# Optimization experiments

Measured on AMD Instinct MI355X. Metric: run time of the kernel, lower is better.

## Reference

```python
import jax, jax.numpy as jnp
import numpy as np

EPS = 0.05
THRESH = 1e-6
MAX_ITER = 100


def _l2norm(x):
    # matches torch F.normalize(dim=-1): x / max(||x||, 1e-12)
    n = jnp.sqrt(jnp.sum(x * x, axis=-1, keepdims=True))
    return x / jnp.maximum(n, 1e-12)


def setup_inputs() -> dict:
    key = jax.random.key(0)
    kq, kk, kv = jax.random.split(key, 3)
    B, N, D = 8, 1024, 64
    return {
        "q": jax.random.normal(kq, (B, N, D), dtype=jnp.float32),
        "k": jax.random.normal(kk, (B, N, D), dtype=jnp.float32),
        "V": jax.random.normal(kv, (B, N, D), dtype=jnp.float32),
    }


def reference(q, k, V):
    B, N, D = q.shape
    Q = _l2norm(q)
    Kn = _l2norm(k)
    # cost matrix: 1 - cosine similarity, shape (B, N, N)
    C = 1.0 - jnp.einsum("bnd,bmd->bnm", Q, Kn)

    log_mu = jnp.full((B, N), jnp.log(1.0 / N + 1e-8), dtype=C.dtype)
    log_nu = log_mu

    def kernel(u, v):
        # (-C + u_i + v_j) / eps, shape (B, N, N)
        return (-C + u[:, :, None] + v[:, None, :]) / EPS

    def step(carry, _):
        u, v, done = carry
        u0 = u
        u_new = EPS * (log_mu - jax.scipy.special.logsumexp(kernel(u, v), axis=2)) + u
        v_new = EPS * (log_nu - jax.scipy.special.logsumexp(kernel(u_new, v), axis=1)) + v
        err = jnp.mean(jnp.abs(u_new - u0))
        # replicate torch early-break: once converged, freeze u, v
        u = jnp.where(done, u, u_new)
        v = jnp.where(done, v, v_new)
        done = jnp.logical_or(done, err < THRESH)
        return (u, v, done), None

    u0 = jnp.zeros((B, N), dtype=C.dtype)
    v0 = jnp.zeros((B, N), dtype=C.dtype)
    (u, v, _), _ = jax.lax.scan(
        jax.checkpoint(step), (u0, v0, jnp.array(False)), None, length=MAX_ITER
    )

    T = jnp.exp(kernel(u, v))  # transport plan (B, N, N)
    out = jnp.einsum("bnm,bmd->bnd", T, V) + V
    return out
```

## Files before the change

### kernel.cpp

```cpp
#include <hip/hip_runtime.h>
#include <math.h>

#define BB 8
#define NN 1024
#define DD 64
#define EPSF 0.05f
#define MAX_ITER 100
#define ERR_SUM_THRESH 8.192e-3f
#define SCALE_ 28.853900817779268f
#define EPSLN2_ 0.034657359027997264f
#define NBLK 256
#define NPER 32

typedef __attribute__((ext_vector_type(8))) short short8;
typedef __attribute__((ext_vector_type(4))) float f32x4;

static __device__ __forceinline__ float fexp2(float x) { return __builtin_amdgcn_exp2f(x); }
static __device__ __forceinline__ float flog2(float x) { return __builtin_amdgcn_logf(x); }
static __device__ __forceinline__ float bflo(unsigned u) { return __uint_as_float(u << 16); }
static __device__ __forceinline__ unsigned short bf16rne(float x) {
    unsigned u = __float_as_uint(x);
    u += 0x7fffu + ((u >> 16) & 1u);
    return (unsigned short)(u >> 16);
}
__device__ __forceinline__ float wave_sum64(float x) {
#pragma unroll
    for (int off = 1; off < 64; off <<= 1) x += __shfl_xor(x, off);
    return x;
}

#define ERRIDX(t, b) ((b) * 128 + (t))
#define CNTIDX(p, b) ((b) * 256 + (p))
#define PUBIDX(t) (t)

__global__ __launch_bounds__(256) void cost_kernel(const float* __restrict__ q,
                                                   const float* __restrict__ k,
                                                   unsigned short* __restrict__ M,
                                                   unsigned short* __restrict__ MT) {
    __shared__ __align__(16) float Qs[64][65];
    __shared__ __align__(16) float Ks[64][65];
    __shared__ float qin[64];
    __shared__ float kin[64];
    __shared__ __align__(16) unsigned short Qb[64][72];
    __shared__ __align__(16) unsigned short Kb[64][72];
    int b = blockIdx.z;
    int i0 = blockIdx.y * 64, j0 = blockIdx.x * 64;
    const float* Qp = q + ((size_t)b * NN + i0) * DD;
    const float* Kp = k + ((size_t)b * NN + j0) * DD;
    int tid = threadIdx.x;
#pragma unroll
    for (int kk = 0; kk < 4; ++kk) {
        int c = tid + 256 * kk;
        int row = c >> 4;
        int c4 = c & 15;
        float4 qv = ((const float4*)(Qp + row * DD))[c4];
        Qs[row][c4 * 4 + 0] = qv.x; Qs[row][c4 * 4 + 1] = qv.y;
        Qs[row][c4 * 4 + 2] = qv.z; Qs[row][c4 * 4 + 3] = qv.w;
        float4 kv = ((const float4*)(Kp + row * DD))[c4];
        Ks[row][c4 * 4 + 0] = kv.x; Ks[row][c4 * 4 + 1] = kv.y;
        Ks[row][c4 * 4 + 2] = kv.z; Ks[row][c4 * 4 + 3] = kv.w;
    }
    __syncthreads();
    if (tid < 64) {
        float ss = 0.f;
#pragma unroll 16
        for (int d = 0; d < 64; ++d) ss += Qs[tid][d] * Qs[tid][d];
        qin[tid] = 1.0f / fmaxf(sqrtf(ss), 1e-12f);
    } else if (tid < 128) {
        int r = tid - 64;
        float ss = 0.f;
#pragma unroll 16
        for (int d = 0; d < 64; ++d) ss += Ks[r][d] * Ks[r][d];
        kin[r] = 1.0f / fmaxf(sqrtf(ss), 1e-12f);
    }
    __syncthreads();
    {
        int row = tid >> 2, d0 = (tid & 3) * 16;
        float qs = qin[row], ks = kin[row];
#pragma unroll
        for (int p = 0; p < 4; ++p) {
            int d = d0 + p * 4;
            uint2 t;
            t.x = (unsigned)bf16rne(Qs[row][d + 0] * qs) | ((unsigned)bf16rne(Qs[row][d + 1] * qs) << 16);
            t.y = (unsigned)bf16rne(Qs[row][d + 2] * qs) | ((unsigned)bf16rne(Qs[row][d + 3] * qs) << 16);
            *(uint2*)&Qb[row][d] = t;
            t.x = (unsigned)bf16rne(Ks[row][d + 0] * ks) | ((unsigned)bf16rne(Ks[row][d + 1] * ks) << 16);
            t.y = (unsigned)bf16rne(Ks[row][d + 2] * ks) | ((unsigned)bf16rne(Ks[row][d + 3] * ks) << 16);
            *(uint2*)&Kb[row][d] = t;
        }
    }
    __syncthreads();
    int w = tid >> 6, lane = tid & 63;
    int m = lane & 15, qq = lane >> 4;
    int rloc = w * 16;
    short8 a0 = *(const short8*)&Qb[rloc + m][qq * 8];
    short8 a1 = *(const short8*)&Qb[rloc + m][qq * 8 + 32];
    f32x4 acc[4];
#pragma unroll
    for (int nt = 0; nt < 4; ++nt) {
        short8 b0 = *(const short8*)&Kb[nt * 16 + m][qq * 8];
        short8 b1 = *(const short8*)&Kb[nt * 16 + m][qq * 8 + 32];
        f32x4 z = {0.f, 0.f, 0.f, 0.f};
        z = __builtin_amdgcn_mfma_f32_16x16x32_bf16(a0, b0, z, 0, 0, 0);
        acc[nt] = __builtin_amdgcn_mfma_f32_16x16x32_bf16(a1, b1, z, 0, 0, 0);
    }
#pragma unroll
    for (int nt = 0; nt < 4; ++nt) {
        int gj = j0 + nt * 16 + m;
        unsigned short us[4];
#pragma unroll
        for (int r = 0; r < 4; ++r)
            us[r] = bf16rne(fexp2((acc[nt][r] - 1.0f) * SCALE_));
#pragma unroll
        for (int r = 0; r < 4; ++r)
            M[((size_t)b << 20) + ((size_t)(i0 + rloc + qq * 4 + r) << 10) + gj] = us[r];
        uint2 t;
        t.x = (unsigned)us[0] | ((unsigned)us[1] << 16);
        t.y = (unsigned)us[2] | ((unsigned)us[3] << 16);
        *(uint2*)(MT + ((size_t)b << 20) + ((size_t)gj << 10) + i0 + rloc + qq * 4) = t;
    }
}

#define ACC8(U4, base)                                              \
    s0 = fmaf(bflo(U4.x), wrg[base + 0], s0);                       \
    s1 = fmaf(__uint_as_float(U4.x), wrg[base + 1], s1);            \
    s0 = fmaf(bflo(U4.y), wrg[base + 2], s0);                       \
    s1 = fmaf(__uint_as_float(U4.y), wrg[base + 3], s1);            \
    s0 = fmaf(bflo(U4.z), wrg[base + 4], s0);                       \
    s1 = fmaf(__uint_as_float(U4.z), wrg[base + 5], s1);            \
    s0 = fmaf(bflo(U4.w), wrg[base + 6], s0);                       \
    s1 = fmaf(__uint_as_float(U4.w), wrg[base + 7], s1);

__global__ __launch_bounds__(256, 1) void sink_coop(const unsigned short* __restrict__ M,
                                                    const unsigned short* __restrict__ MT,
                                                    float* __restrict__ u,
                                                    float* __restrict__ v,
                                                    float* __restrict__ err,
                                                    unsigned* __restrict__ cnt,
                                                    unsigned* __restrict__ pub,
                                                    float eln) {
    __shared__ __align__(16) float sw[1280];
    __shared__ float sdel[4];
    __shared__ int sflag;
    int tid = threadIdx.x;
    int w = tid >> 6, lane = tid & 63;
    int b = blockIdx.x & 7;
    int slice = blockIdx.x >> 3;
    int rbase = slice * 32 + w * 8;
    const unsigned short* Mb  = M  + ((size_t)b << 20);
    const unsigned short* MTb = MT + ((size_t)b << 20);
    float* ub = u + (b << 10);
    float* vb = v + (b << 10);

    uint4 mA[8], mB[8], nA[8], nB[8];
#pragma unroll
    for (int r = 0; r < 8; ++r) {
        const uint4* rp = (const uint4*)(Mb + ((size_t)(rbase + r) << 10));
        mA[r] = rp[lane * 2];
        mB[r] = rp[lane * 2 + 1];
        const uint4* tp = (const uint4*)(MTb + ((size_t)(rbase + r) << 10));
        nA[r] = tp[lane * 2];
        nB[r] = tp[lane * 2 + 1];
    }

    float uprev[8];
#pragma unroll
    for (int r = 0; r < 8; ++r) uprev[r] = 0.f;

    for (int t = 0; t < MAX_ITER; ++t) {
        {
            float4 ex;
            ex.x = fexp2(__hip_atomic_load(vb + tid * 4 + 0, __ATOMIC_RELAXED, __HIP_MEMORY_SCOPE_AGENT) * SCALE_);
            ex.y = fexp2(__hip_atomic_load(vb + tid * 4 + 1, __ATOMIC_RELAXED, __HIP_MEMORY_SCOPE_AGENT) * SCALE_);
            ex.z = fexp2(__hip_atomic_load(vb + tid * 4 + 2, __ATOMIC_RELAXED, __HIP_MEMORY_SCOPE_AGENT) * SCALE_);
            ex.w = fexp2(__hip_atomic_load(vb + tid * 4 + 3, __ATOMIC_RELAXED, __HIP_MEMORY_SCOPE_AGENT) * SCALE_);
            *(float4*)&sw[tid * 4 + 4 * (tid >> 2)] = ex;
            __syncthreads();
            float wrg[16];
            *(float4*)&wrg[0]  = *(const float4*)&sw[lane * 20 + 0];
            *(float4*)&wrg[4]  = *(const float4*)&sw[lane * 20 + 4];
            *(float4*)&wrg[8]  = *(const float4*)&sw[lane * 20 + 8];
            *(float4*)&wrg[12] = *(const float4*)&sw[lane * 20 + 12];
            float del = 0.f;
#pragma unroll
            for (int rr = 0; rr < 8; ++rr) {
                float s0 = 0.f, s1 = 0.f;
                ACC8(mA[rr], 0)
                ACC8(mB[rr], 8)
                float s = wave_sum64(s0 + s1);
                float un = eln - EPSLN2_ * flog2(s);
                del += fabsf(un - uprev[rr]);
                uprev[rr] = un;
                if (lane == 0)
                    __hip_atomic_store(ub + rbase + rr, un, __ATOMIC_RELAXED, __HIP_MEMORY_SCOPE_AGENT);
            }
            if (lane == 0) sdel[w] = del;
            asm volatile("s_waitcnt vmcnt(0)" ::: "memory");
            __syncthreads();
            if (tid == 0) {
                __hip_atomic_fetch_add(err + ERRIDX(t, b), sdel[0] + sdel[1] + sdel[2] + sdel[3],
                                       __ATOMIC_RELAXED, __HIP_MEMORY_SCOPE_AGENT);
                asm volatile("s_waitcnt vmcnt(0)" ::: "memory");
                unsigned* c = cnt + CNTIDX(2 * t, b);
                __hip_atomic_fetch_add(c, 1u, __ATOMIC_RELAXED, __HIP_MEMORY_SCOPE_AGENT);
                while (__hip_atomic_load(c, __ATOMIC_RELAXED, __HIP_MEMORY_SCOPE_AGENT) < NPER)
                    __builtin_amdgcn_s_sleep(1);
                if (slice == 0) {
                    asm volatile("s_waitcnt vmcnt(0)" ::: "memory");
                    __hip_atomic_fetch_add(pub + PUBIDX(t), 1u, __ATOMIC_RELAXED, __HIP_MEMORY_SCOPE_AGENT);
                }
            }
            __syncthreads();
        }
        {
            float4 ex;
            ex.x = fexp2(__hip_atomic_load(ub + tid * 4 + 0, __ATOMIC_RELAXED, __HIP_MEMORY_SCOPE_AGENT) * SCALE_);
            ex.y = fexp2(__hip_atomic_load(ub + tid * 4 + 1, __ATOMIC_RELAXED, __HIP_MEMORY_SCOPE_AGENT) * SCALE_);
            ex.z = fexp2(__hip_atomic_load(ub + tid * 4 + 2, __ATOMIC_RELAXED, __HIP_MEMORY_SCOPE_AGENT) * SCALE_);
            ex.w = fexp2(__hip_atomic_load(ub + tid * 4 + 3, __ATOMIC_RELAXED, __HIP_MEMORY_SCOPE_AGENT) * SCALE_);
            *(float4*)&sw[tid * 4 + 4 * (tid >> 2)] = ex;
            __syncthreads();
            float wrg[16];
            *(float4*)&wrg[0]  = *(const float4*)&sw[lane * 20 + 0];
            *(float4*)&wrg[4]  = *(const float4*)&sw[lane * 20 + 4];
            *(float4*)&wrg[8]  = *(const float4*)&sw[lane * 20 + 8];
            *(float4*)&wrg[12] = *(const float4*)&sw[lane * 20 + 12];
#pragma unroll
            for (int rr = 0; rr < 8; ++rr) {
                float s0 = 0.f, s1 = 0.f;
                ACC8(nA[rr], 0)
                ACC8(nB[rr], 8)
                float s = wave_sum64(s0 + s1);
                float vn = eln - EPSLN2_ * flog2(s);
                if (lane == 0)
                    __hip_atomic_store(vb + rbase + rr, vn, __ATOMIC_RELAXED, __HIP_MEMORY_SCOPE_AGENT);
            }
            asm volatile("s_waitcnt vmcnt(0)" ::: "memory");
            __syncthreads();
            if (tid == 0) {
                unsigned* c = cnt + CNTIDX(2 * t + 1, b);
                __hip_atomic_fetch_add(c, 1u, __ATOMIC_RELAXED, __HIP_MEMORY_SCOPE_AGENT);
                while (__hip_atomic_load(c, __ATOMIC_RELAXED, __HIP_MEMORY_SCOPE_AGENT) < NPER)
                    __builtin_amdgcn_s_sleep(1);
                float eb = __hip_atomic_load(err + ERRIDX(t, b), __ATOMIC_RELAXED, __HIP_MEMORY_SCOPE_AGENT);
                int brk = 0;
                if (eb < ERR_SUM_THRESH) {
                    while (__hip_atomic_load(pub + PUBIDX(t), __ATOMIC_RELAXED, __HIP_MEMORY_SCOPE_AGENT) < 8u)
                        __builtin_amdgcn_s_sleep(1);
                    float s = 0.f;
                    for (int bb = 0; bb < 8; ++bb)
                        s += __hip_atomic_load(err + ERRIDX(t, bb), __ATOMIC_RELAXED, __HIP_MEMORY_SCOPE_AGENT);
                    brk = (s < ERR_SUM_THRESH);
                }
                sflag = brk;
            }
            __syncthreads();
            if (sflag) break;
        }
    }
}

__global__ __launch_bounds__(256) void wt_kernel(const float* __restrict__ V,
                                                 const float* __restrict__ v,
                                                 unsigned short* __restrict__ WT) {
    __shared__ __align__(16) float Vs[64][65];
    __shared__ float wj[64];
    int b = blockIdx.x & 7, jt = blockIdx.x >> 3;
    int j0 = jt * 64;
    int tid = threadIdx.x;
    const float* Vb = V + ((size_t)b << 16) + ((size_t)j0 << 6);
#pragma unroll
    for (int c = 0; c < 4; ++c) {
        int idx = tid + 256 * c;
        int row = idx >> 4, c4 = idx & 15;
        float4 x = ((const float4*)(Vb + row * 64))[c4];
        Vs[row][c4 * 4 + 0] = x.x; Vs[row][c4 * 4 + 1] = x.y;
        Vs[row][c4 * 4 + 2] = x.z; Vs[row][c4 * 4 + 3] = x.w;
    }
    if (tid < 64) wj[tid] = fexp2(v[(b << 10) + j0 + tid] * SCALE_);
    __syncthreads();
    int d = tid >> 2, qd = tid & 3;
    unsigned pk[8];
#pragma unroll
    for (int p = 0; p < 8; ++p) {
        int j = qd * 16 + p * 2;
        unsigned lo = bf16rne(Vs[j][d] * wj[j]);
        unsigned hi = bf16rne(Vs[j + 1][d] * wj[j + 1]);
        pk[p] = lo | (hi << 16);
    }
    unsigned short* dst = WT + ((size_t)b << 16) + ((size_t)d << 10) + j0 + qd * 16;
    ((uint4*)dst)[0] = make_uint4(pk[0], pk[1], pk[2], pk[3]);
    ((uint4*)dst)[1] = make_uint4(pk[4], pk[5], pk[6], pk[7]);
}

__global__ __launch_bounds__(256) void gemm_final(const unsigned short* __restrict__ M,
                                                  const unsigned short* __restrict__ WT,
                                                  const float* __restrict__ u,
                                                  const float* __restrict__ V,
                                                  float* __restrict__ out) {
    __shared__ float sa[32];
    int tid = threadIdx.x;
    int w = tid >> 6, lane = tid & 63;
    int b = blockIdx.x & 7, mt = blockIdx.x >> 3;
    if (tid < 32) sa[tid] = fexp2(u[(b << 10) + mt * 32 + tid] * SCALE_);
    __syncthreads();
    int m = lane & 15, q = lane >> 4;
    int rloc = (w & 1) * 16;
    int nbase = (w >> 1) * 32;
    const unsigned short* Ma = M + ((size_t)b << 20) + ((size_t)(mt * 32 + rloc + m) << 10) + q * 8;
    const unsigned short* W0 = WT + ((size_t)b << 16) + ((size_t)(nbase + m) << 10) + q * 8;
    const unsigned short* W1 = W0 + (16 << 10);
    f32x4 acc0 = {0.f, 0.f, 0.f, 0.f}, acc1 = {0.f, 0.f, 0.f, 0.f};
#pragma unroll 4
    for (int k0 = 0; k0 < NN; k0 += 32) {
        short8 af = *(const short8*)(Ma + k0);
        short8 b0 = *(const short8*)(W0 + k0);
        short8 b1 = *(const short8*)(W1 + k0);
        acc0 = __builtin_amdgcn_mfma_f32_16x16x32_bf16(af, b0, acc0, 0, 0, 0);
        acc1 = __builtin_amdgcn_mfma_f32_16x16x32_bf16(af, b1, acc1, 0, 0, 0);
    }
#pragma unroll
    for (int r = 0; r < 4; ++r) {
        int lrow = rloc + q * 4 + r;
        int gm = mt * 32 + lrow;
        float a = sa[lrow];
        size_t base = (((size_t)b << 10) + gm) * DD;
        int n0 = nbase + m;
        out[base + n0]      = fmaf(a, acc0[r], V[base + n0]);
        out[base + n0 + 16] = fmaf(a, acc1[r], V[base + n0 + 16]);
    }
}

extern "C" void kernel_launch(void* const* d_in, const int* in_sizes, int n_in,
                              void* d_out, int out_size, void* d_ws, size_t ws_size,
                              hipStream_t stream) {
    const float* q = (const float*)d_in[0];
    const float* k = (const float*)d_in[1];
    const float* V = (const float*)d_in[2];
    float* out = (float*)d_out;

    char* ws = (char*)d_ws;
    const size_t MB16 = (size_t)BB * NN * NN * sizeof(unsigned short);
    unsigned short* M  = (unsigned short*)ws;
    unsigned short* MT = (unsigned short*)(ws + MB16);
    unsigned short* WT = MT;
    float* u   = (float*)(ws + 2 * MB16);
    float* v   = u + BB * NN;
    float* err = v + BB * NN;
    unsigned* cnt = (unsigned*)(err + 1024);
    unsigned* pub = cnt + 2048;

    size_t zbytes = (size_t)(2 * BB * NN + 1024 + 2048 + 128) * 4;
    hipMemsetAsync(u, 0, zbytes, stream);

    cost_kernel<<<dim3(16, 16, 8), 256, 0, stream>>>(q, k, M, MT);

    float eln = EPSF * logf(1.0f / NN + 1e-8f);
    sink_coop<<<dim3(NBLK), dim3(256), 0, stream>>>(M, MT, u, v, err, cnt, pub, eln);

    wt_kernel<<<128, 256, 0, stream>>>(V, v, WT);
    gemm_final<<<256, 256, 0, stream>>>(M, WT, u, V, out);
}
```

Measured before the change: 196.3 us.

## Pack barrier count and fixed-point error into one 64-bit atomic, coalesce M stores

The per-iteration grid barrier in the Sinkhorn loop now packs the arrival count and a fixed-point error sum into a single 64-bit atomic. This removes the separate error atomic, its waitcnt, and the publish counter, so the convergence check reads per-batch totals directly from the barrier words. The cost kernel also stages the M tile in shared memory and writes it out with coalesced 16-byte stores instead of scattered 2-byte stores. The fixed-point quantisation of the error (scaled by 2^20, plus 1 per block) slightly changes the break threshold semantics.

```diff
diff --git a/kernel.cpp b/kernel.cpp
--- a/kernel.cpp
+++ b/kernel.cpp
@@ -6,7 +6,7 @@
 #define DD 64
 #define EPSF 0.05f
 #define MAX_ITER 100
-#define ERR_SUM_THRESH 8.192e-3f
+#define ERR_FX_THRESH 8590u
 #define SCALE_ 28.853900817779268f
 #define EPSLN2_ 0.034657359027997264f
 #define NBLK 256
@@ -29,9 +29,7 @@
     return x;
 }
 
-#define ERRIDX(t, b) ((b) * 128 + (t))
-#define CNTIDX(p, b) ((b) * 256 + (p))
-#define PUBIDX(t) (t)
+#define CNT64IDX(p, b) ((b) * 200 + (p))
 
 __global__ __launch_bounds__(256) void cost_kernel(const float* __restrict__ q,
                                                    const float* __restrict__ k,
@@ -90,6 +88,7 @@
         }
     }
     __syncthreads();
+    unsigned short* Ms = (unsigned short*)&Qs[0][0];
     int w = tid >> 6, lane = tid & 63;
     int m = lane & 15, qq = lane >> 4;
     int rloc = w * 16;
@@ -113,11 +112,19 @@
             us[r] = bf16rne(fexp2((acc[nt][r] - 1.0f) * SCALE_));
 #pragma unroll
         for (int r = 0; r < 4; ++r)
-            M[((size_t)b << 20) + ((size_t)(i0 + rloc + qq * 4 + r) << 10) + gj] = us[r];
+            Ms[(rloc + qq * 4 + r) * 72 + nt * 16 + m] = us[r];
         uint2 t;
         t.x = (unsigned)us[0] | ((unsigned)us[1] << 16);
         t.y = (unsigned)us[2] | ((unsigned)us[3] << 16);
         *(uint2*)(MT + ((size_t)b << 20) + ((size_t)gj << 10) + i0 + rloc + qq * 4) = t;
+    }
+    __syncthreads();
+#pragma unroll
+    for (int s = 0; s < 2; ++s) {
+        int idx = tid + 256 * s;
+        int row = idx >> 3, seg = idx & 7;
+        *(uint4*)(M + ((size_t)b << 20) + ((size_t)(i0 + row) << 10) + j0 + seg * 8) =
+            *(const uint4*)&Ms[row * 72 + seg * 8];
     }
 }
 
@@ -135,9 +142,7 @@
                                                     const unsigned short* __restrict__ MT,
                                                     float* __restrict__ u,
                                                     float* __restrict__ v,
-                                                    float* __restrict__ err,
-                                                    unsigned* __restrict__ cnt,
-                                                    unsigned* __restrict__ pub,
+                                                    unsigned long long* __restrict__ cnt64,
                                                     float eln) {
     __shared__ __align__(16) float sw[1280];
     __shared__ float sdel[4];
@@ -167,6 +172,8 @@
 #pragma unroll
     for (int r = 0; r < 8; ++r) uprev[r] = 0.f;
 
+    unsigned myerr = 0xffffffffu;
+
     for (int t = 0; t < MAX_ITER; ++t) {
         {
             float4 ex;
@@ -198,17 +205,18 @@
             asm volatile("s_waitcnt vmcnt(0)" ::: "memory");
             __syncthreads();
             if (tid == 0) {
-                __hip_atomic_fetch_add(err + ERRIDX(t, b), sdel[0] + sdel[1] + sdel[2] + sdel[3],
-                                       __ATOMIC_RELAXED, __HIP_MEMORY_SCOPE_AGENT);
-                asm volatile("s_waitcnt vmcnt(0)" ::: "memory");
-                unsigned* c = cnt + CNTIDX(2 * t, b);
-                __hip_atomic_fetch_add(c, 1u, __ATOMIC_RELAXED, __HIP_MEMORY_SCOPE_AGENT);
-                while (__hip_atomic_load(c, __ATOMIC_RELAXED, __HIP_MEMORY_SCOPE_AGENT) < NPER)
+                float dsum = sdel[0] + sdel[1] + sdel[2] + sdel[3];
+                unsigned dfx = (unsigned)fminf(dsum * 1048576.0f, 6.0e7f) + 1u;
+                unsigned long long* c = cnt64 + CNT64IDX(2 * t, b);
+                unsigned long long tot =
+                    __hip_atomic_fetch_add(c, (1ULL << 32) | (unsigned long long)dfx,
+                                           __ATOMIC_RELAXED, __HIP_MEMORY_SCOPE_AGENT) +
+                    ((1ULL << 32) | (unsigned long long)dfx);
+                while ((unsigned)(tot >> 32) < NPER) {
                     __builtin_amdgcn_s_sleep(1);
-                if (slice == 0) {
-                    asm volatile("s_waitcnt vmcnt(0)" ::: "memory");
-                    __hip_atomic_fetch_add(pub + PUBIDX(t), 1u, __ATOMIC_RELAXED, __HIP_MEMORY_SCOPE_AGENT);
+                    tot = __hip_atomic_load(c, __ATOMIC_RELAXED, __HIP_MEMORY_SCOPE_AGENT);
                 }
+                myerr = (unsigned)tot;
             }
             __syncthreads();
         }
@@ -238,19 +246,28 @@
             asm volatile("s_waitcnt vmcnt(0)" ::: "memory");
             __syncthreads();
             if (tid == 0) {
-                unsigned* c = cnt + CNTIDX(2 * t + 1, b);
-                __hip_atomic_fetch_add(c, 1u, __ATOMIC_RELAXED, __HIP_MEMORY_SCOPE_AGENT);
-                while (__hip_atomic_load(c, __ATOMIC_RELAXED, __HIP_MEMORY_SCOPE_AGENT) < NPER)
+                unsigned long long* c = cnt64 + CNT64IDX(2 * t + 1, b);
+                unsigned long long tot =
+                    __hip_atomic_fetch_add(c, 1ULL << 32, __ATOMIC_RELAXED, __HIP_MEMORY_SCOPE_AGENT) +
+                    (1ULL << 32);
+                while ((unsigned)(tot >> 32) < NPER) {
                     __builtin_amdgcn_s_sleep(1);
-                float eb = __hip_atomic_load(err + ERRIDX(t, b), __ATOMIC_RELAXED, __HIP_MEMORY_SCOPE_AGENT);
+                    tot = __hip_atomic_load(c, __ATOMIC_RELAXED, __HIP_MEMORY_SCOPE_AGENT);
+                }
                 int brk = 0;
-                if (eb < ERR_SUM_THRESH) {
-                    while (__hip_atomic_load(pub + PUBIDX(t), __ATOMIC_RELAXED, __HIP_MEMORY_SCOPE_AGENT) < 8u)
-                        __builtin_amdgcn_s_sleep(1);
-                    float s = 0.f;
-                    for (int bb = 0; bb < 8; ++bb)
-                        s += __hip_atomic_load(err + ERRIDX(t, bb), __ATOMIC_RELAXED, __HIP_MEMORY_SCOPE_AGENT);
-                    brk = (s < ERR_SUM_THRESH);
+                if (myerr < ERR_FX_THRESH) {
+                    unsigned long long s = 0;
+                    for (int bb = 0; bb < 8; ++bb) {
+                        unsigned long long tv = __hip_atomic_load(cnt64 + CNT64IDX(2 * t, bb),
+                                                                  __ATOMIC_RELAXED, __HIP_MEMORY_SCOPE_AGENT);
+                        while ((unsigned)(tv >> 32) < NPER) {
+                            __builtin_amdgcn_s_sleep(1);
+                            tv = __hip_atomic_load(cnt64 + CNT64IDX(2 * t, bb),
+                                                   __ATOMIC_RELAXED, __HIP_MEMORY_SCOPE_AGENT);
+                        }
+                        s += (unsigned long long)(unsigned)tv;
+                    }
+                    brk = (s < (unsigned long long)ERR_FX_THRESH);
                 }
                 sflag = brk;
             }
@@ -346,17 +363,15 @@
     unsigned short* WT = MT;
     float* u   = (float*)(ws + 2 * MB16);
     float* v   = u + BB * NN;
-    float* err = v + BB * NN;
-    unsigned* cnt = (unsigned*)(err + 1024);
-    unsigned* pub = cnt + 2048;
-
-    size_t zbytes = (size_t)(2 * BB * NN + 1024 + 2048 + 128) * 4;
+    unsigned long long* cnt64 = (unsigned long long*)(v + BB * NN);
+
+    size_t zbytes = (size_t)(2 * BB * NN) * 4 + 1600 * 8;
     hipMemsetAsync(u, 0, zbytes, stream);
 
     cost_kernel<<<dim3(16, 16, 8), 256, 0, stream>>>(q, k, M, MT);
 
     float eln = EPSF * logf(1.0f / NN + 1e-8f);
-    sink_coop<<<dim3(NBLK), dim3(256), 0, stream>>>(M, MT, u, v, err, cnt, pub, eln);
+    sink_coop<<<dim3(NBLK), dim3(256), 0, stream>>>(M, MT, u, v, cnt64, eln);
 
     wt_kernel<<<128, 256, 0, stream>>>(V, v, WT);
     gemm_final<<<256, 256, 0, stream>>>(M, WT, u, V, out);
```

Result: faster. 183.8 us (-6.4%).
